# Optimization experiments

Hardware: AMD Instinct MI355X
Metric: run time of the kernel (lower is better)

## Reference

```python
import jax, jax.numpy as jnp
import numpy as np

MAGBIAS = 0.01
INV_SQRT2 = np.float32(1.0 / np.sqrt(2.0))


def _reflect(x, minx, maxx):
    # Half-sample symmetric reflection of indices (static numpy; matches dtcwt reflect()).
    rng = maxx - minx
    mod = np.fmod(x - minx, 2.0 * rng)
    mod = np.where(mod < 0, mod + 2.0 * rng, mod)
    out = np.where(mod >= rng, 2.0 * rng - mod, mod) + minx
    return np.round(out).astype(np.int64)


def _symm_pad(l, m):
    return _reflect(np.arange(-m, l + m, dtype=np.float64), -0.5, l - 0.5)


def _depthwise(X, h, axis, stride):
    # Per-channel 1-D correlation along rows (axis=2) or cols (axis=3), NCHW, like F.conv2d(groups=ch).
    ch = X.shape[1]
    if axis == 2:
        k = h.reshape(1, 1, -1, 1)
        strides = (stride, 1)
    else:
        k = h.reshape(1, 1, 1, -1)
        strides = (1, stride)
    k = jnp.tile(k, (ch, 1, 1, 1)).astype(X.dtype)
    return jax.lax.conv_general_dilated(
        X, k, window_strides=strides, padding='VALID',
        dimension_numbers=('NCHW', 'OIHW', 'NCHW'), feature_group_count=ch)


def colfilter(X, h):
    m = h.shape[0] // 2
    xe = _symm_pad(X.shape[2], m)
    return _depthwise(X[:, :, xe, :], h, axis=2, stride=1)


def rowfilter(X, h):
    m = h.shape[0] // 2
    xe = _symm_pad(X.shape[3], m)
    return _depthwise(X[:, :, :, xe], h, axis=3, stride=1)


def coldfilt(X, ha, hb, highpass):
    # Dual-tree decimated column filtering with a quarter-shift pair; output rows = r // 2.
    b, ch, r, c = X.shape
    m = ha.shape[0]
    xe = _symm_pad(r, m)
    ya = _depthwise(X[:, :, xe[2::2], :], ha, axis=2, stride=2)  # (b,ch,r/4,c)
    yb = _depthwise(X[:, :, xe[3::2], :], hb, axis=2, stride=2)
    first, second = (yb, ya) if highpass else (ya, yb)
    return jnp.stack([first, second], axis=3).reshape(b, ch, r // 2, c)


def rowdfilt(X, ha, hb, highpass):
    b, ch, r, c = X.shape
    m = ha.shape[0]
    xe = _symm_pad(c, m)
    ya = _depthwise(X[:, :, :, xe[2::2]], ha, axis=3, stride=2)
    yb = _depthwise(X[:, :, :, xe[3::2]], hb, axis=3, stride=2)
    first, second = (yb, ya) if highpass else (ya, yb)
    return jnp.stack([first, second], axis=4).reshape(b, ch, r, c // 2)


def q2c(y):
    # Quads -> two complex subbands (real, imag): the DTCWT butterfly combine.
    y = y * INV_SQRT2
    a = y[..., 0::2, 0::2]
    b = y[..., 0::2, 1::2]
    c = y[..., 1::2, 0::2]
    d = y[..., 1::2, 1::2]
    return (a - d, b + c), (a + d, b - c)


def _stack_orients(lh, hl, hh):
    (d15r, d15i), (d165r, d165i) = q2c(lh)
    (d45r, d45i), (d135r, d135i) = q2c(hh)
    (d75r, d75i), (d105r, d105i) = q2c(hl)
    reals = jnp.stack([d15r, d45r, d75r, d105r, d135r, d165r], axis=1)
    imags = jnp.stack([d15i, d45i, d75i, d105i, d135i, d165i], axis=1)
    return reals, imags


def fwd_j1(x, h0, h1):
    # Level-1 DTCWT: undecimated separable biorthogonal filters + q2c.
    lo = rowfilter(x, h0)
    hi = rowfilter(x, h1)
    ll = colfilter(lo, h0)
    lh = colfilter(lo, h1)
    hl = colfilter(hi, h0)
    hh = colfilter(hi, h1)
    reals, imags = _stack_orients(lh, hl, hh)
    return ll, reals, imags


def fwd_j2plus(x, h0a, h1a, h0b, h1b):
    # Level-2 DTCWT: decimated quarter-shift filter pairs + q2c.
    lo = rowdfilt(x, h0b, h0a, False)
    hi = rowdfilt(x, h1b, h1a, True)
    ll = coldfilt(lo, h0b, h0a, False)
    lh = coldfilt(lo, h1b, h1a, True)
    hl = coldfilt(hi, h0b, h0a, False)
    hh = coldfilt(hi, h1b, h1a, True)
    reals, imags = _stack_orients(lh, hl, hh)
    return ll, reals, imags


def _smooth_mag(re, im, bias):
    return jnp.sqrt(re * re + im * im + bias * bias) - bias


def _avgpool2(x):
    b, ch, r, c = x.shape
    return x.reshape(b, ch, r // 2, 2, c // 2, 2).mean(axis=(3, 5))


def _scat_forward(x, h0o, h1o, h0a, h0b, h1a, h1b):
    b, ch, r, c = x.shape  # r, c multiples of 8 (input already padded)
    # First order, scale j=1
    ll, re, im = fwd_j1(x, h0o, h1o)
    s1_j1 = _smooth_mag(re, im, MAGBIAS)                      # (b,6,ch,r/2,c/2)
    # First order, scale j=2 (on the running lowpass)
    ll, re, im = fwd_j2plus(ll, h0a, h1a, h0b, h1b)           # ll: (b,ch,r/2,c/2)
    s1_j2 = _smooth_mag(re, im, MAGBIAS)                      # (b,6,ch,r/4,c/4)
    # Second order: one more octave on the first-order magnitudes
    p = s1_j1.reshape(b, 6 * ch, r // 2, c // 2)
    p, re, im = fwd_j1(p, h0o, h1o)
    s2 = _smooth_mag(re, im, MAGBIAS).reshape(b, 36, ch, r // 4, c // 4)
    s0 = _avgpool2(ll)[:, None]                               # (b,1,ch,r/4,c/4)
    s1_j1 = _avgpool2(p).reshape(b, 6, ch, r // 4, c // 4)
    Z = jnp.concatenate([s0, s1_j1, s1_j2, s2], axis=1)       # (b,49,ch,r/4,c/4)
    return Z.reshape(b, 49 * ch, r // 4, c // 4)


def setup_inputs():
    key = jax.random.key(0)
    ks = jax.random.split(key, 5)
    x = jax.random.normal(ks[0], (32, 3, 512, 512), dtype=jnp.float32)
    h0o = jax.random.normal(ks[1], (5,), dtype=jnp.float32) * 0.3
    h1o = jax.random.normal(ks[2], (7,), dtype=jnp.float32) * 0.3
    h0a = jax.random.normal(ks[3], (10,), dtype=jnp.float32) * 0.3
    h1a = jax.random.normal(ks[4], (10,), dtype=jnp.float32) * 0.3
    h0b = h0a[::-1]  # quarter-shift pair: time-reverse of the tree-a filter
    h1b = h1a[::-1]
    return {"x": x, "h0o": h0o, "h1o": h1o, "h0a": h0a, "h0b": h0b,
            "h1a": h1a, "h1b": h1b}


def reference(x, h0o, h1o, h0a, h0b, h1a, h1b):
    return _scat_forward(x, h0o, h1o, h0a, h0b, h1a, h1b)
```

## Files before the change

kernel.cpp:

```cpp
#include <hip/hip_runtime.h>

#define IS2 0.70710678118654752440f

__device__ __forceinline__ int refl(int i, int n) {
    if (i < 0) i = -1 - i;
    if (i >= n) i = 2 * n - 1 - i;
    return i;
}

__device__ __forceinline__ float smag(float re, float im) {
    return sqrtf(re * re + im * im + 1.0e-4f) - 0.01f;
}

template <int MODE>
__device__ __forceinline__
void j1_tile(float* __restrict__ smem,
             const float* __restrict__ in,
             const float* __restrict__ h0,
             const float* __restrict__ h1,
             float* __restrict__ ll_out,
             float* __restrict__ mag_out,
             int CH, int N, int img, int ty0, int tx0)
{
    const int b   = img / CH;
    const int chn = img % CH;
    const int tid = threadIdx.x;

    float* const sx  = smem;
    float* const slo = smem + 5040;
    float* const shi = sx;

    float f0[5], f1[7];
#pragma unroll
    for (int t = 0; t < 5; ++t) f0[t] = h0[t];
#pragma unroll
    for (int t = 0; t < 7; ++t) f1[t] = h1[t];

    const float* src = in + (size_t)img * N * N;

    for (int e = tid; e < 70 * 70; e += 256) {
        int rr = e / 70, cc = e % 70;
        int gr = refl(ty0 - 3 + rr, N);
        int gc = refl(tx0 - 3 + cc, N);
        sx[rr * 72 + cc] = src[(size_t)gr * N + gc];
    }
    __syncthreads();

    float rlo[5][4], rhi[5][4];
#pragma unroll
    for (int k = 0; k < 5; ++k) {
        int e = tid + k * 256;
        if (e < 1120) {
            int rr = e >> 4, g = e & 15;
            const float4* w4 = (const float4*)&sx[rr * 72 + 4 * g];
            float4 wa = w4[0], wb = w4[1], wc = w4[2];
            float win[12] = {wa.x, wa.y, wa.z, wa.w,
                             wb.x, wb.y, wb.z, wb.w,
                             wc.x, wc.y, wc.z, wc.w};
#pragma unroll
            for (int u = 0; u < 4; ++u) {
                float lo = 0.f, hi = 0.f;
#pragma unroll
                for (int t = 0; t < 5; ++t) lo += win[u + 1 + t] * f0[t];
#pragma unroll
                for (int t = 0; t < 7; ++t) hi += win[u + t] * f1[t];
                rlo[k][u] = lo; rhi[k][u] = hi;
            }
        }
    }
    __syncthreads();
#pragma unroll
    for (int k = 0; k < 5; ++k) {
        int e = tid + k * 256;
        if (e < 1120) {
            int rr = e >> 4, g = e & 15;
            *(float4*)&slo[rr * 64 + 4 * g] =
                make_float4(rlo[k][0], rlo[k][1], rlo[k][2], rlo[k][3]);
            *(float4*)&shi[rr * 64 + 4 * g] =
                make_float4(rhi[k][0], rhi[k][1], rhi[k][2], rhi[k][3]);
        }
    }
    __syncthreads();

    const int j     = tid & 63;
    const int rg    = tid >> 6;
    const int rbase = rg * 16;

    float clo[22], chi[22];
#pragma unroll
    for (int t = 0; t < 22; ++t) {
        clo[t] = slo[(rbase + t) * 64 + j];
        chi[t] = shi[(rbase + t) * 64 + j];
    }

    const int Nh  = N >> 1;
    const int par = j & 1;
    const int qx  = (tx0 >> 1) + (j >> 1);
    const int qy0 = (ty0 >> 1) + rg * 8;
    const int oLH = par ? 5 : 0;
    const int oHH = par ? 4 : 1;
    const int oHL = par ? 3 : 2;

    float* lcol = nullptr;
    float* pLH = nullptr; float* pHH = nullptr; float* pHL = nullptr;
    float* zBase = nullptr;
    size_t zLH = 0, zHH = 0, zHL = 0, zPL = 0;
    if (MODE == 0) {
        lcol = ll_out + (size_t)img * N * N + (size_t)(ty0 + rbase) * N + tx0 + j;
        const size_t planeSz = (size_t)Nh * Nh;
        const size_t qoff = (size_t)qy0 * Nh + qx;
        pLH = mag_out + ((size_t)(b * 6 + oLH) * CH + chn) * planeSz + qoff;
        pHH = mag_out + ((size_t)(b * 6 + oHH) * CH + chn) * planeSz + qoff;
        pHL = mag_out + ((size_t)(b * 6 + oHL) * CH + chn) * planeSz + qoff;
    } else {
        const int o1 = chn / 3, c3 = chn % 3;
        zBase = mag_out + (size_t)b * 147 * 16384 + (size_t)qy0 * 128 + qx;
        zLH = (size_t)((13 + oLH * 6 + o1) * 3 + c3) * 16384;
        zHH = (size_t)((13 + oHH * 6 + o1) * 3 + c3) * 16384;
        zHL = (size_t)((13 + oHL * 6 + o1) * 3 + c3) * 16384;
        zPL = (size_t)((1 + o1) * 3 + c3) * 16384;
    }

#pragma unroll
    for (int ii = 0; ii < 8; ++ii) {
        const int i0 = 2 * ii, i1 = 2 * ii + 1;
        float ll0 = 0.f, ll1 = 0.f, lh0 = 0.f, lh1 = 0.f;
        float hl0 = 0.f, hl1 = 0.f, hh0 = 0.f, hh1 = 0.f;
#pragma unroll
        for (int t = 0; t < 5; ++t) {
            ll0 += clo[i0 + 1 + t] * f0[t]; ll1 += clo[i1 + 1 + t] * f0[t];
            hl0 += chi[i0 + 1 + t] * f0[t]; hl1 += chi[i1 + 1 + t] * f0[t];
        }
#pragma unroll
        for (int t = 0; t < 7; ++t) {
            lh0 += clo[i0 + t] * f1[t]; lh1 += clo[i1 + t] * f1[t];
            hh0 += chi[i0 + t] * f1[t]; hh1 += chi[i1 + t] * f1[t];
        }

        float lhT = __shfl_xor(lh0, 1), lhB = __shfl_xor(lh1, 1);
        float hhT = __shfl_xor(hh0, 1), hhB = __shfl_xor(hh1, 1);
        float hlT = __shfl_xor(hl0, 1), hlB = __shfl_xor(hl1, 1);
        float mLH = smag(IS2 * (lh0 - lhB), IS2 * (lhT + lh1));
        float mHH = smag(IS2 * (hh0 - hhB), IS2 * (hhT + hh1));
        float mHL = smag(IS2 * (hl0 - hlB), IS2 * (hlT + hl1));

        if (MODE == 0) {
            lcol[(size_t)i0 * N] = ll0;
            lcol[(size_t)i1 * N] = ll1;
            pLH[(size_t)ii * Nh] = mLH;
            pHH[(size_t)ii * Nh] = mHH;
            pHL[(size_t)ii * Nh] = mHL;
        } else {
            float* zr = zBase + (size_t)ii * 128;
            zr[zLH] = mLH;
            zr[zHH] = mHH;
            zr[zHL] = mHL;
            float llT = __shfl_xor(ll0, 1), llB = __shfl_xor(ll1, 1);
            if (par == 0) {
                zr[zPL] = 0.25f * (ll0 + ll1 + llT + llB);
            }
        }
    }
}

__device__ __forceinline__
void j2_tile(float* __restrict__ smem,
             const float* __restrict__ ll,
             const float* __restrict__ h0a, const float* __restrict__ h0b,
             const float* __restrict__ h1a, const float* __restrict__ h1b,
             float* __restrict__ Z, int img, int r0, int c0)
{
    const int b = img / 3, c = img % 3;
    const int tid = threadIdx.x;

    float* const sx   = smem;
    float* const sloP = sx;
    float* const shiP = sx + 2688;

    float fa0[10], fb0[10], fa1[10], fb1[10];
#pragma unroll
    for (int t = 0; t < 10; ++t) {
        fa0[t] = h0a[t]; fb0[t] = h0b[t];
        fa1[t] = h1a[t]; fb1[t] = h1b[t];
    }

    const float* src = ll + (size_t)img * 512 * 512;

    for (int e = tid; e < 80 * 80; e += 256) {
        int rr = e / 80, cc = e % 80;
        int gr = refl(2 * r0 - 8 + rr, 512);
        int gc = refl(2 * c0 - 8 + cc, 512);
        sx[rr * 84 + cc] = src[(size_t)gr * 512 + gc];
    }
    __syncthreads();

    const int jj  = tid & 31;
    const int odd = jj & 1;
    const int base = 2 * (jj & ~1);
    float hlo[10], hhi[10];
#pragma unroll
    for (int t = 0; t < 10; ++t) {
        hlo[t] = odd ? fa0[t] : fb0[t];
        hhi[t] = odd ? fb1[t] : fa1[t];
    }
    const int offlo = base + odd;
    const int offhi = base + 1 - odd;
    float rlo[10], rhi[10];
#pragma unroll
    for (int k = 0; k < 10; ++k) {
        int rr = (tid >> 5) + 8 * k;
        const float* row = &sx[rr * 84];
        float lo = 0.f, hi = 0.f;
#pragma unroll
        for (int t = 0; t < 10; ++t) {
            lo += row[offlo + 2 * t] * hlo[t];
            hi += row[offhi + 2 * t] * hhi[t];
        }
        rlo[k] = lo; rhi[k] = hi;
    }
    __syncthreads();
#pragma unroll
    for (int k = 0; k < 10; ++k) {
        int rr = (tid >> 5) + 8 * k;
        sloP[rr * 33 + jj] = rlo[k];
        shiP[rr * 33 + jj] = rhi[k];
    }
    __syncthreads();

    const int qi = tid >> 4, qj = tid & 15;
    float ll2[2][2], lh4[2][2], hl4[2][2], hh4[2][2];
#pragma unroll
    for (int dj = 0; dj < 2; ++dj) {
        const int col = 2 * qj + dj;
        const int rb  = 4 * qi;
        float vll0 = 0.f, vll1 = 0.f, vlh0 = 0.f, vlh1 = 0.f;
        float vhl0 = 0.f, vhl1 = 0.f, vhh0 = 0.f, vhh1 = 0.f;
#pragma unroll
        for (int t = 0; t < 10; ++t) {
            float e0 = sloP[(rb + 2 * t) * 33 + col];
            float e1 = sloP[(rb + 2 * t + 1) * 33 + col];
            float g0 = shiP[(rb + 2 * t) * 33 + col];
            float g1 = shiP[(rb + 2 * t + 1) * 33 + col];
            vll0 += e0 * fb0[t];
            vll1 += e1 * fa0[t];
            vlh0 += e1 * fa1[t];
            vlh1 += e0 * fb1[t];
            vhl0 += g0 * fb0[t];
            vhl1 += g1 * fa0[t];
            vhh0 += g1 * fa1[t];
            vhh1 += g0 * fb1[t];
        }
        ll2[0][dj] = vll0; ll2[1][dj] = vll1;
        lh4[0][dj] = vlh0; lh4[1][dj] = vlh1;
        hl4[0][dj] = vhl0; hl4[1][dj] = vhl1;
        hh4[0][dj] = vhh0; hh4[1][dj] = vhh1;
    }

    const int qy = (r0 >> 1) + qi;
    const int qx = (c0 >> 1) + qj;
    float* Zb = Z + (size_t)b * 147 * 16384 + (size_t)qy * 128 + qx;

    Zb[(size_t)c * 16384] =
        0.25f * (ll2[0][0] + ll2[0][1] + ll2[1][0] + ll2[1][1]);

    {
        float a, bq, cq, d;
        float m[6];
        a = lh4[0][0] * IS2; bq = lh4[0][1] * IS2; cq = lh4[1][0] * IS2; d = lh4[1][1] * IS2;
        m[0] = smag(a - d, bq + cq); m[5] = smag(a + d, bq - cq);
        a = hh4[0][0] * IS2; bq = hh4[0][1] * IS2; cq = hh4[1][0] * IS2; d = hh4[1][1] * IS2;
        m[1] = smag(a - d, bq + cq); m[4] = smag(a + d, bq - cq);
        a = hl4[0][0] * IS2; bq = hl4[0][1] * IS2; cq = hl4[1][0] * IS2; d = hl4[1][1] * IS2;
        m[2] = smag(a - d, bq + cq); m[3] = smag(a + d, bq - cq);
#pragma unroll
        for (int o = 0; o < 6; ++o) {
            Zb[(size_t)((7 + o) * 3 + c) * 16384] = m[o];
        }
    }
}

__global__ __launch_bounds__(256, 4)
void k_j1_l1(const float* __restrict__ x,
             const float* __restrict__ h0o, const float* __restrict__ h1o,
             float* __restrict__ ll, float* __restrict__ p)
{
    __shared__ __align__(16) float smem[9520];
    j1_tile<0>(smem, x, h0o, h1o, ll, p, 3, 512,
               blockIdx.z, blockIdx.y * 64, blockIdx.x * 64);
}

__global__ __launch_bounds__(256, 4)
void k_p23(const float* __restrict__ ll, const float* __restrict__ p,
           const float* __restrict__ h0o, const float* __restrict__ h1o,
           const float* __restrict__ h0a, const float* __restrict__ h0b,
           const float* __restrict__ h1a, const float* __restrict__ h1b,
           float* __restrict__ Z)
{
    __shared__ __align__(16) float smem[9520];
    const int B = blockIdx.x;
    if (B < 6144) {
        const int img = B >> 6, rem = B & 63;
        j2_tile(smem, ll, h0a, h0b, h1a, h1b, Z,
                img, ((rem >> 3) & 7) * 32, (rem & 7) * 32);
    } else {
        const int T = B - 6144;
        const int img = T >> 4, rem = T & 15;
        j1_tile<1>(smem, p, h0o, h1o, nullptr, Z, 18, 256,
                   img, ((rem >> 2) & 3) * 64, (rem & 3) * 64);
    }
}

extern "C" void kernel_launch(void* const* d_in, const int* in_sizes, int n_in,
                              void* d_out, int out_size, void* d_ws, size_t ws_size,
                              hipStream_t stream)
{
    const float* x   = (const float*)d_in[0];
    const float* h0o = (const float*)d_in[1];
    const float* h1o = (const float*)d_in[2];
    const float* h0a = (const float*)d_in[3];
    const float* h0b = (const float*)d_in[4];
    const float* h1a = (const float*)d_in[5];
    const float* h1b = (const float*)d_in[6];
    float* Z = (float*)d_out;

    float* ws_ll = (float*)d_ws;
    float* ws_p  = ws_ll + (size_t)32 * 3 * 512 * 512;

    dim3 blk(256);
    k_j1_l1<<<dim3(8, 8, 96), blk, 0, stream>>>(x, h0o, h1o, ws_ll, ws_p);
    k_p23<<<dim3(15360), blk, 0, stream>>>(ws_ll, ws_p, h0o, h1o,
                                           h0a, h0b, h1a, h1b, Z);
}
```

Baseline: 590.3 us.

## Vectorize interior tile loads, template sizes, restructure j2 column pass with shuffles

```diff
diff --git a/kernel.cpp b/kernel.cpp
--- a/kernel.cpp
+++ b/kernel.cpp
@@ -12,7 +12,7 @@
     return sqrtf(re * re + im * im + 1.0e-4f) - 0.01f;
 }
 
-template <int MODE>
+template <int MODE, int N, int CH>
 __device__ __forceinline__
 void j1_tile(float* __restrict__ smem,
              const float* __restrict__ in,
@@ -20,7 +20,7 @@
              const float* __restrict__ h1,
              float* __restrict__ ll_out,
              float* __restrict__ mag_out,
-             int CH, int N, int img, int ty0, int tx0)
+             int img, int ty0, int tx0)
 {
     const int b   = img / CH;
     const int chn = img % CH;
@@ -38,11 +38,22 @@
 
     const float* src = in + (size_t)img * N * N;
 
-    for (int e = tid; e < 70 * 70; e += 256) {
-        int rr = e / 70, cc = e % 70;
-        int gr = refl(ty0 - 3 + rr, N);
-        int gc = refl(tx0 - 3 + cc, N);
-        sx[rr * 72 + cc] = src[(size_t)gr * N + gc];
+    const bool interior = (ty0 >= 3) && (ty0 + 66 <= N - 1) &&
+                          (tx0 >= 4) && (tx0 + 67 <= N - 1);
+    if (interior) {
+        const float* bp = src + (size_t)(ty0 - 3) * N + (tx0 - 4);
+        for (int e = tid; e < 70 * 18; e += 256) {
+            int rr = e / 18, g = e - rr * 18;
+            *(float4*)&sx[rr * 72 + 4 * g] =
+                *(const float4*)(bp + (size_t)rr * N + 4 * g);
+        }
+    } else {
+        for (int e = tid; e < 70 * 72; e += 256) {
+            int rr = e / 72, cc = e - rr * 72;
+            int gr = refl(ty0 - 3 + rr, N);
+            int gc = refl(tx0 - 4 + cc, N);
+            sx[rr * 72 + cc] = src[(size_t)gr * N + gc];
+        }
     }
     __syncthreads();
 
@@ -61,9 +72,9 @@
             for (int u = 0; u < 4; ++u) {
                 float lo = 0.f, hi = 0.f;
 #pragma unroll
-                for (int t = 0; t < 5; ++t) lo += win[u + 1 + t] * f0[t];
-#pragma unroll
-                for (int t = 0; t < 7; ++t) hi += win[u + t] * f1[t];
+                for (int t = 0; t < 5; ++t) lo += win[u + 2 + t] * f0[t];
+#pragma unroll
+                for (int t = 0; t < 7; ++t) hi += win[u + 1 + t] * f1[t];
                 rlo[k][u] = lo; rhi[k][u] = hi;
             }
         }
@@ -103,8 +114,8 @@
 
     float* lcol = nullptr;
     float* pLH = nullptr; float* pHH = nullptr; float* pHL = nullptr;
-    float* zBase = nullptr;
-    size_t zLH = 0, zHH = 0, zHL = 0, zPL = 0;
+    float* zLH = nullptr; float* zHH = nullptr; float* zHL = nullptr;
+    float* zPL = nullptr;
     if (MODE == 0) {
         lcol = ll_out + (size_t)img * N * N + (size_t)(ty0 + rbase) * N + tx0 + j;
         const size_t planeSz = (size_t)Nh * Nh;
@@ -114,11 +125,11 @@
         pHL = mag_out + ((size_t)(b * 6 + oHL) * CH + chn) * planeSz + qoff;
     } else {
         const int o1 = chn / 3, c3 = chn % 3;
-        zBase = mag_out + (size_t)b * 147 * 16384 + (size_t)qy0 * 128 + qx;
-        zLH = (size_t)((13 + oLH * 6 + o1) * 3 + c3) * 16384;
-        zHH = (size_t)((13 + oHH * 6 + o1) * 3 + c3) * 16384;
-        zHL = (size_t)((13 + oHL * 6 + o1) * 3 + c3) * 16384;
-        zPL = (size_t)((1 + o1) * 3 + c3) * 16384;
+        float* zBase = mag_out + (size_t)b * 147 * 16384 + (size_t)qy0 * 128 + qx;
+        zLH = zBase + (size_t)((13 + oLH * 6 + o1) * 3 + c3) * 16384;
+        zHH = zBase + (size_t)((13 + oHH * 6 + o1) * 3 + c3) * 16384;
+        zHL = zBase + (size_t)((13 + oHL * 6 + o1) * 3 + c3) * 16384;
+        zPL = zBase + (size_t)((1 + o1) * 3 + c3) * 16384;
     }
 
 #pragma unroll
@@ -147,17 +158,17 @@
         if (MODE == 0) {
             lcol[(size_t)i0 * N] = ll0;
             lcol[(size_t)i1 * N] = ll1;
-            pLH[(size_t)ii * Nh] = mLH;
-            pHH[(size_t)ii * Nh] = mHH;
-            pHL[(size_t)ii * Nh] = mHL;
+            pLH[ii * Nh] = mLH;
+            pHH[ii * Nh] = mHH;
+            pHL[ii * Nh] = mHL;
         } else {
-            float* zr = zBase + (size_t)ii * 128;
-            zr[zLH] = mLH;
-            zr[zHH] = mHH;
-            zr[zHL] = mHL;
+            __builtin_nontemporal_store(mLH, zLH + ii * 128);
+            __builtin_nontemporal_store(mHH, zHH + ii * 128);
+            __builtin_nontemporal_store(mHL, zHL + ii * 128);
             float llT = __shfl_xor(ll0, 1), llB = __shfl_xor(ll1, 1);
             if (par == 0) {
-                zr[zPL] = 0.25f * (ll0 + ll1 + llT + llB);
+                __builtin_nontemporal_store(
+                    0.25f * (ll0 + ll1 + llT + llB), zPL + ii * 128);
             }
         }
     }
@@ -185,12 +196,24 @@
     }
 
     const float* src = ll + (size_t)img * 512 * 512;
-
-    for (int e = tid; e < 80 * 80; e += 256) {
-        int rr = e / 80, cc = e % 80;
-        int gr = refl(2 * r0 - 8 + rr, 512);
-        int gc = refl(2 * c0 - 8 + cc, 512);
-        sx[rr * 84 + cc] = src[(size_t)gr * 512 + gc];
+    const int gy0 = 2 * r0 - 8, gx0 = 2 * c0 - 8;
+
+    const bool interior = (gy0 >= 0) && (gy0 + 79 <= 511) &&
+                          (gx0 >= 0) && (gx0 + 79 <= 511);
+    if (interior) {
+        const float* bp = src + (size_t)gy0 * 512 + gx0;
+        for (int e = tid; e < 80 * 20; e += 256) {
+            int rr = e / 20, g = e - rr * 20;
+            *(float4*)&sx[rr * 84 + 4 * g] =
+                *(const float4*)(bp + (size_t)rr * 512 + 4 * g);
+        }
+    } else {
+        for (int e = tid; e < 80 * 80; e += 256) {
+            int rr = e / 80, cc = e - rr * 80;
+            int gr = refl(gy0 + rr, 512);
+            int gc = refl(gx0 + cc, 512);
+            sx[rr * 84 + cc] = src[(size_t)gr * 512 + gc];
+        }
     }
     __syncthreads();
 
@@ -227,20 +250,40 @@
     }
     __syncthreads();
 
-    const int qi = tid >> 4, qj = tid & 15;
-    float ll2[2][2], lh4[2][2], hl4[2][2], hh4[2][2];
-#pragma unroll
-    for (int dj = 0; dj < 2; ++dj) {
-        const int col = 2 * qj + dj;
-        const int rb  = 4 * qi;
+    const int j = tid & 31;
+    const int g = tid >> 5;
+
+    float clo[24], chi[24];
+#pragma unroll
+    for (int t = 0; t < 24; ++t) {
+        clo[t] = sloP[(8 * g + t) * 33 + j];
+        chi[t] = shiP[(8 * g + t) * 33 + j];
+    }
+
+    const int dj  = j & 1;
+    const int qx  = (c0 >> 1) + (j >> 1);
+    const int qy0 = (r0 >> 1) + 2 * g;
+    const int oLH = dj ? 5 : 0;
+    const int oHH = dj ? 4 : 1;
+    const int oHL = dj ? 3 : 2;
+
+    float* Zb = Z + (size_t)b * 147 * 16384 + (size_t)qy0 * 128 + qx;
+    float* zLH = Zb + (size_t)((7 + oLH) * 3 + c) * 16384;
+    float* zHH = Zb + (size_t)((7 + oHH) * 3 + c) * 16384;
+    float* zHL = Zb + (size_t)((7 + oHL) * 3 + c) * 16384;
+    float* zPL = Zb + (size_t)c * 16384;
+
+#pragma unroll
+    for (int r = 0; r < 2; ++r) {
+        const int off = 4 * r;
         float vll0 = 0.f, vll1 = 0.f, vlh0 = 0.f, vlh1 = 0.f;
         float vhl0 = 0.f, vhl1 = 0.f, vhh0 = 0.f, vhh1 = 0.f;
 #pragma unroll
         for (int t = 0; t < 10; ++t) {
-            float e0 = sloP[(rb + 2 * t) * 33 + col];
-            float e1 = sloP[(rb + 2 * t + 1) * 33 + col];
-            float g0 = shiP[(rb + 2 * t) * 33 + col];
-            float g1 = shiP[(rb + 2 * t + 1) * 33 + col];
+            float e0 = clo[off + 2 * t];
+            float e1 = clo[off + 2 * t + 1];
+            float g0 = chi[off + 2 * t];
+            float g1 = chi[off + 2 * t + 1];
             vll0 += e0 * fb0[t];
             vll1 += e1 * fa0[t];
             vlh0 += e1 * fa1[t];
@@ -250,31 +293,22 @@
             vhh0 += g1 * fa1[t];
             vhh1 += g0 * fb1[t];
         }
-        ll2[0][dj] = vll0; ll2[1][dj] = vll1;
-        lh4[0][dj] = vlh0; lh4[1][dj] = vlh1;
-        hl4[0][dj] = vhl0; hl4[1][dj] = vhl1;
-        hh4[0][dj] = vhh0; hh4[1][dj] = vhh1;
-    }
-
-    const int qy = (r0 >> 1) + qi;
-    const int qx = (c0 >> 1) + qj;
-    float* Zb = Z + (size_t)b * 147 * 16384 + (size_t)qy * 128 + qx;
-
-    Zb[(size_t)c * 16384] =
-        0.25f * (ll2[0][0] + ll2[0][1] + ll2[1][0] + ll2[1][1]);
-
-    {
-        float a, bq, cq, d;
-        float m[6];
-        a = lh4[0][0] * IS2; bq = lh4[0][1] * IS2; cq = lh4[1][0] * IS2; d = lh4[1][1] * IS2;
-        m[0] = smag(a - d, bq + cq); m[5] = smag(a + d, bq - cq);
-        a = hh4[0][0] * IS2; bq = hh4[0][1] * IS2; cq = hh4[1][0] * IS2; d = hh4[1][1] * IS2;
-        m[1] = smag(a - d, bq + cq); m[4] = smag(a + d, bq - cq);
-        a = hl4[0][0] * IS2; bq = hl4[0][1] * IS2; cq = hl4[1][0] * IS2; d = hl4[1][1] * IS2;
-        m[2] = smag(a - d, bq + cq); m[3] = smag(a + d, bq - cq);
-#pragma unroll
-        for (int o = 0; o < 6; ++o) {
-            Zb[(size_t)((7 + o) * 3 + c) * 16384] = m[o];
+
+        float lhT = __shfl_xor(vlh0, 1), lhB = __shfl_xor(vlh1, 1);
+        float hhT = __shfl_xor(vhh0, 1), hhB = __shfl_xor(vhh1, 1);
+        float hlT = __shfl_xor(vhl0, 1), hlB = __shfl_xor(vhl1, 1);
+        float mLH = smag(IS2 * (vlh0 - lhB), IS2 * (lhT + vlh1));
+        float mHH = smag(IS2 * (vhh0 - hhB), IS2 * (hhT + vhh1));
+        float mHL = smag(IS2 * (vhl0 - hlB), IS2 * (hlT + vhl1));
+
+        __builtin_nontemporal_store(mLH, zLH + r * 128);
+        __builtin_nontemporal_store(mHH, zHH + r * 128);
+        __builtin_nontemporal_store(mHL, zHL + r * 128);
+
+        float llT = __shfl_xor(vll0, 1), llB = __shfl_xor(vll1, 1);
+        if (dj == 0) {
+            __builtin_nontemporal_store(
+                0.25f * (vll0 + vll1 + llT + llB), zPL + r * 128);
         }
     }
 }
@@ -285,8 +319,8 @@
              float* __restrict__ ll, float* __restrict__ p)
 {
     __shared__ __align__(16) float smem[9520];
-    j1_tile<0>(smem, x, h0o, h1o, ll, p, 3, 512,
-               blockIdx.z, blockIdx.y * 64, blockIdx.x * 64);
+    j1_tile<0, 512, 3>(smem, x, h0o, h1o, ll, p,
+                       blockIdx.z, blockIdx.y * 64, blockIdx.x * 64);
 }
 
 __global__ __launch_bounds__(256, 4)
@@ -305,8 +339,8 @@
     } else {
         const int T = B - 6144;
         const int img = T >> 4, rem = T & 15;
-        j1_tile<1>(smem, p, h0o, h1o, nullptr, Z, 18, 256,
-                   img, ((rem >> 2) & 3) * 64, (rem & 3) * 64);
+        j1_tile<1, 256, 18>(smem, p, h0o, h1o, nullptr, Z,
+                            img, ((rem >> 2) & 3) * 64, (rem & 3) * 64);
     }
 }
 
```

Result: faster. 562.1 us (-4.8%).
